# Performance work log

Measured on AMD Instinct MI355X. Metric: run time of the kernel, lower is better.

The kernel has to match this reference:

```python
import jax, jax.numpy as jnp
import numpy as np

E1 = 150000   # number of 1-hop edges
E2 = 150000   # number of 2-hop edges
T = 400000    # triangles per triangle class
C = 64        # in_channels
H = 64        # mlp_hidden_channels
L = 2         # num DR2FWL2Conv layers
N_MLP = 8     # MLPs per conv layer


def setup_inputs() -> dict:
    key = jax.random.key(0)
    ks = jax.random.split(key, 20)
    edge_attr = jax.random.normal(ks[0], (E1, C), jnp.float32)
    edge_attr2 = jax.random.normal(ks[1], (E2, C), jnp.float32)
    # triangle index tensors: rows (ij, ik, kj); hop type of each row decides the range
    triangle_1_1_1 = jax.random.randint(ks[2], (3, T), 0, E1)
    triangle_1_1_2 = jnp.stack([jax.random.randint(jax.random.fold_in(ks[3], r), (T,), 0, m)
                                for r, m in enumerate([E1, E1, E2])])
    triangle_1_2_2 = jnp.stack([jax.random.randint(jax.random.fold_in(ks[4], r), (T,), 0, m)
                                for r, m in enumerate([E1, E2, E2])])
    triangle_2_2_2 = jax.random.randint(ks[5], (3, T), 0, E2)
    inverse_edge_1 = jax.random.permutation(ks[6], E1)
    inverse_edge_2 = jax.random.permutation(ks[7], E2)
    s = 0.05
    mlp_w1 = jax.random.normal(ks[8], (L, N_MLP, C, H), jnp.float32) * s
    mlp_b1 = jnp.zeros((L, N_MLP, H), jnp.float32)
    mlp_w2 = jax.random.normal(ks[9], (L, N_MLP, H, C), jnp.float32) * s
    mlp_b2 = jnp.zeros((L, N_MLP, C), jnp.float32)
    lin_w1 = jax.random.normal(ks[10], (C, C), jnp.float32) * s
    lin_b1 = jnp.zeros((C,), jnp.float32)
    lin_w2 = jax.random.normal(ks[11], (C, C), jnp.float32) * s
    lin_b2 = jnp.zeros((C,), jnp.float32)
    return dict(edge_attr=edge_attr, edge_attr2=edge_attr2,
                triangle_1_1_1=triangle_1_1_1, triangle_1_1_2=triangle_1_1_2,
                triangle_1_2_2=triangle_1_2_2, triangle_2_2_2=triangle_2_2_2,
                inverse_edge_1=inverse_edge_1, inverse_edge_2=inverse_edge_2,
                mlp_w1=mlp_w1, mlp_b1=mlp_b1, mlp_w2=mlp_w2, mlp_b2=mlp_b2,
                lin_w1=lin_w1, lin_b1=lin_b1, lin_w2=lin_w2, lin_b2=lin_b2)


def reference(edge_attr, edge_attr2, triangle_1_1_1, triangle_1_1_2,
              triangle_1_2_2, triangle_2_2_2, inverse_edge_1, inverse_edge_2,
              mlp_w1, mlp_b1, mlp_w2, mlp_b2, lin_w1, lin_b1, lin_w2, lin_b2):
    eps = 0.0
    eps2 = 0.0
    ij111, ik111, kj111 = triangle_1_1_1
    ij112, ik112, kj112 = triangle_1_1_2
    ij122, ik122, kj122 = triangle_1_2_2
    ij222, ik222, kj222 = triangle_2_2_2
    seg = jax.ops.segment_sum

    e1, e2 = edge_attr, edge_attr2
    n1, n2 = e1.shape[0], e2.shape[0]
    for li in range(mlp_w1.shape[0]):
        def mlp(x, mi, li=li):
            h = jax.nn.relu(x @ mlp_w1[li, mi] + mlp_b1[li, mi])
            return h @ mlp_w2[li, mi] + mlp_b2[li, mi]
        m111 = seg(mlp(e1[ik111], 0) * mlp(e1[kj111], 0), ij111, num_segments=n1)
        m112 = seg(mlp(e1[ik112], 1) * mlp(e2[kj112], 2), ij112, num_segments=n1)
        m122 = seg(mlp(e2[ik122], 3) * mlp(e2[kj122], 3), ij122, num_segments=n1)
        e1 = e1 * (1.0 + eps) + m111 + m112 + m112[inverse_edge_1] + m122
        m211 = seg(mlp(e1[ij112], 4) * mlp(e1[ik112], 4), kj112, num_segments=n2)
        m212 = seg(mlp(e1[ij122], 5) * mlp(e2[kj122], 6), ik122, num_segments=n2)
        m222 = seg(mlp(e2[ik222], 7) * mlp(e2[kj222], 7), ij222, num_segments=n2)
        e2 = e2 * (1.0 + eps2) + m211 + m212 + m212[inverse_edge_2] + m222
        # norm=None (Identity), relu after, dropout=0 in eval
        e1, e2 = jax.nn.relu(e1), jax.nn.relu(e2)
    return (e1 @ lin_w1 + lin_b1, e2 @ lin_w2 + lin_b2)
```

## Files before the change

kernel.cpp:

```cpp
#include <hip/hip_runtime.h>
#include <hip/hip_fp16.h>


typedef unsigned short u16;
typedef unsigned int u32;
typedef _Float16 f16;
typedef __attribute__((ext_vector_type(8))) short s16x8;
typedef __attribute__((ext_vector_type(4))) float f32x4;
typedef __attribute__((ext_vector_type(8))) _Float16 f16x8;

#define MFMA16(a, b, c) __builtin_amdgcn_mfma_f32_16x16x32_bf16((a), (b), (c), 0, 0, 0)

static __device__ __forceinline__ u16 bf16_rne(float x) {
  u32 u = __float_as_uint(x);
  return (u16)((u + 0x7fffu + ((u >> 16) & 1u)) >> 16);
}
static __device__ __forceinline__ float bf16_f32(u16 h) {
  return __uint_as_float(((u32)h) << 16);
}
static __device__ __forceinline__ void cvt_hilo8_f16(const f16x8 v, s16x8& hi, s16x8& lo) {
#pragma unroll
  for (int j = 0; j < 8; j++) {
    float x = (float)v[j];
    u16 h = bf16_rne(x);
    hi[j] = (short)h;
    lo[j] = (short)bf16_rne(x - bf16_f32(h));
  }
}

__global__ __launch_bounds__(256) void repack_split_kernel(const float* __restrict__ src,
                                                           u16* __restrict__ hi, u16* __restrict__ lo, int nmat) {
  int o = blockIdx.x * 256 + threadIdx.x;
  int stride = gridDim.x * 256;
  int total = nmat * 4096;
  for (; o < total; o += stride) {
    int m = o >> 12, r = o & 4095;
    int j = r & 7, lane = (r >> 3) & 63, nt = (r >> 9) & 3, kt = (r >> 11) & 1;
    int k = kt * 32 + ((lane >> 4) << 3) + j;
    int n = nt * 16 + (lane & 15);
    float x = src[(size_t)m * 4096 + k * 64 + n];
    u16 h = bf16_rne(x);
    hi[o] = h;
    lo[o] = bf16_rne(x - bf16_f32(h));
  }
}

__global__ __launch_bounds__(256) void cvtcopy_kernel(const float* __restrict__ src, f16* __restrict__ dst, int n8) {
  int i = blockIdx.x * 256 + threadIdx.x;
  int stride = gridDim.x * 256;
  const f32x4* s4 = (const f32x4*)src;
  f16x8* d8 = (f16x8*)dst;
  for (; i < n8; i += stride) {
    f32x4 a = s4[2 * i], b = s4[2 * i + 1];
    f16x8 o;
#pragma unroll
    for (int j = 0; j < 4; j++) { o[j] = (f16)a[j]; o[4 + j] = (f16)b[j]; }
    d8[i] = o;
  }
}

__global__ __launch_bounds__(256) void relu16_kernel(f16* __restrict__ e, int n8) {
  int i = blockIdx.x * 256 + threadIdx.x;
  int stride = gridDim.x * 256;
  f16x8* e8 = (f16x8*)e;
  for (; i < n8; i += stride) {
    f16x8 v = e8[i];
#pragma unroll
    for (int j = 0; j < 8; j++) v[j] = v[j] > (f16)0 ? v[j] : (f16)0;
    e8[i] = v;
  }
}

template <bool DO_RELU>
__global__ __launch_bounds__(256) void addinvB_kernel(f16* __restrict__ e, const f16* __restrict__ B,
                                                      const int* __restrict__ inv, int E) {
  int i = blockIdx.x * 256 + threadIdx.x;
  int stride = gridDim.x * 256;
  int total = E * 8;
  f16x8* e8 = (f16x8*)e;
  const f16x8* B8 = (const f16x8*)B;
  for (; i < total; i += stride) {
    int r = i >> 3, q = i & 7;
    int ir = inv[r];
    f16x8 ev = e8[i];
    f16x8 bv = B8[i];
    f16x8 biv = B8[(size_t)ir * 8 + q];
#pragma unroll
    for (int j = 0; j < 8; j++) {
      float x = (float)ev[j] + (float)bv[j] + (float)biv[j];
      ev[j] = (f16)(DO_RELU ? fmaxf(x, 0.0f) : x);
    }
    e8[i] = ev;
  }
}

__global__ __launch_bounds__(256) void seg3_kernel(
    __half2* __restrict__ dstA, __half2* __restrict__ dstB,
    const __half2* __restrict__ paA, const __half2* __restrict__ pbA,
    const int* __restrict__ iA0, const int* __restrict__ iA1, const int* __restrict__ iA2,
    const __half2* __restrict__ paB, const __half2* __restrict__ pbB,
    const int* __restrict__ iB0, const int* __restrict__ iB1, const int* __restrict__ iB2,
    const __half2* __restrict__ paC, const __half2* __restrict__ pbC,
    const int* __restrict__ iC0, const int* __restrict__ iC1, const int* __restrict__ iC2,
    int T) {
  int i = blockIdx.x * 256 + threadIdx.x;
  int stride = gridDim.x * 256;
  int total = 3 * T * 32;
  for (; i < total; i += stride) {
    int u = i >> 5, cp = i & 31;
    __half2* dst;
    const __half2 *pa, *pb;
    const int *i0, *i1, *i2;
    int t;
    if (u < T) { t = u; dst = dstA; pa = paA; pb = pbA; i0 = iA0; i1 = iA1; i2 = iA2; }
    else if (u < 2 * T) { t = u - T; dst = dstB; pa = paB; pb = pbB; i0 = iB0; i1 = iB1; i2 = iB2; }
    else { t = u - 2 * T; dst = dstA; pa = paC; pb = pbC; i0 = iC0; i1 = iC1; i2 = iC2; }
    __half2 va = pa[(size_t)i1[t] * 32 + cp];
    __half2 vb = pb[(size_t)i2[t] * 32 + cp];
    float2 fa = __half22float2(va), fb = __half22float2(vb);
    __half2 prod = __floats2half2_rn(fa.x * fb.x, fa.y * fb.y);
    unsafeAtomicAdd(&dst[(size_t)i0[t] * 32 + cp], prod);
  }
}

__global__ __launch_bounds__(256) void mlpN_kernel(
    const f16* __restrict__ e1s, const f16* __restrict__ e2s,
    f16* __restrict__ d0, f16* __restrict__ d1, f16* __restrict__ d2,
    f16* __restrict__ d3, f16* __restrict__ d4, f16* __restrict__ d5,
    const u16* __restrict__ w1h_, const u16* __restrict__ w1l_,
    const u16* __restrict__ w2h_, const u16* __restrict__ w2l_,
    const float* __restrict__ b1_, const float* __restrict__ b2_,
    int miPacked, int selMask, int nUnits, int s1, int s2, int BPU) {
  __shared__ float hshm[4][1024];
  const int u = blockIdx.x / BPU;
  if (u >= nUnits) return;
  const int tid = threadIdx.x;
  const int wave = tid >> 6, lane = tid & 63;
  const int lrow = lane & 15, lk = lane >> 4;

  const int mi = (miPacked >> (4 * u)) & 15;
  const int sel = (selMask >> u) & 1;
  const f16* src = sel ? e2s : e1s;
  const int strips = sel ? s2 : s1;
  f16* dst = (u == 0) ? d0 : (u == 1) ? d1 : (u == 2) ? d2 : (u == 3) ? d3 : (u == 4) ? d4 : d5;

  const s16x8* W1H = (const s16x8*)(w1h_ + (size_t)mi * 4096);
  const s16x8* W1L = (const s16x8*)(w1l_ + (size_t)mi * 4096);
  const s16x8* W2H = (const s16x8*)(w2h_ + (size_t)mi * 4096);
  const s16x8* W2L = (const s16x8*)(w2l_ + (size_t)mi * 4096);
  s16x8 w1h[2][4], w1l[2][4], w2h[2][4], w2l[2][4];
#pragma unroll
  for (int kt = 0; kt < 2; kt++)
#pragma unroll
    for (int nt = 0; nt < 4; nt++) {
      const int f = (kt * 4 + nt) * 64 + lane;
      w1h[kt][nt] = W1H[f];
      w1l[kt][nt] = W1L[f];
      w2h[kt][nt] = W2H[f];
      w2l[kt][nt] = W2L[f];
    }
  float bias1[4], bias2[4];
#pragma unroll
  for (int nt = 0; nt < 4; nt++) {
    bias1[nt] = b1_[mi * 64 + nt * 16 + lrow];
    bias2[nt] = b2_[mi * 64 + nt * 16 + lrow];
  }

  float* hl = hshm[wave];
  const int lb = blockIdx.x % BPU;
  for (int strip = lb * 4 + wave; strip < strips; strip += BPU * 4) {
    const f16* xp = src + (size_t)(strip * 16 + lrow) * 64 + lk * 8;
    f16x8 xa = *(const f16x8*)(xp);
    f16x8 xb = *(const f16x8*)(xp + 32);
    s16x8 ah[2], al[2];
    cvt_hilo8_f16(xa, ah[0], al[0]);
    cvt_hilo8_f16(xb, ah[1], al[1]);

    f32x4 acc[4];
#pragma unroll
    for (int nt = 0; nt < 4; nt++) { acc[nt][0] = bias1[nt]; acc[nt][1] = bias1[nt]; acc[nt][2] = bias1[nt]; acc[nt][3] = bias1[nt]; }
#pragma unroll
    for (int kt = 0; kt < 2; kt++)
#pragma unroll
      for (int nt = 0; nt < 4; nt++) {
        acc[nt] = MFMA16(ah[kt], w1h[kt][nt], acc[nt]);
        acc[nt] = MFMA16(ah[kt], w1l[kt][nt], acc[nt]);
        acc[nt] = MFMA16(al[kt], w1h[kt][nt], acc[nt]);
      }

#pragma unroll
    for (int nt = 0; nt < 4; nt++)
#pragma unroll
      for (int r = 0; r < 4; r++) {
        const int row = lk * 4 + r;
        const int col = nt * 16 + lrow;
        hl[row * 64 + (col ^ ((row & 7) << 2))] = fmaxf(acc[nt][r], 0.0f);
      }
    s16x8 bh[2], bl[2];
#pragma unroll
    for (int kt = 0; kt < 2; kt++) {
      const int colb = kt * 32 + lk * 8;
      const int xr = (lrow & 7) << 2;
      f32x4 h0 = *(const f32x4*)&hl[lrow * 64 + ((colb + 0) ^ xr)];
      f32x4 h1 = *(const f32x4*)&hl[lrow * 64 + ((colb + 4) ^ xr)];
      s16x8 hi, lo;
#pragma unroll
      for (int j = 0; j < 4; j++) {
        float x = h0[j];
        u16 h = bf16_rne(x);
        hi[j] = (short)h; lo[j] = (short)bf16_rne(x - bf16_f32(h));
      }
#pragma unroll
      for (int j = 0; j < 4; j++) {
        float x = h1[j];
        u16 h = bf16_rne(x);
        hi[4 + j] = (short)h; lo[4 + j] = (short)bf16_rne(x - bf16_f32(h));
      }
      bh[kt] = hi; bl[kt] = lo;
    }

    f32x4 out[4];
#pragma unroll
    for (int nt = 0; nt < 4; nt++) { out[nt][0] = bias2[nt]; out[nt][1] = bias2[nt]; out[nt][2] = bias2[nt]; out[nt][3] = bias2[nt]; }
#pragma unroll
    for (int kt = 0; kt < 2; kt++)
#pragma unroll
      for (int nt = 0; nt < 4; nt++) {
        out[nt] = MFMA16(bh[kt], w2h[kt][nt], out[nt]);
        out[nt] = MFMA16(bh[kt], w2l[kt][nt], out[nt]);
        out[nt] = MFMA16(bl[kt], w2h[kt][nt], out[nt]);
      }

    f16* dp = dst + (size_t)strip * 1024;
#pragma unroll
    for (int nt = 0; nt < 4; nt++)
#pragma unroll
      for (int r = 0; r < 4; r++)
        dp[(lk * 4 + r) * 64 + nt * 16 + lrow] = (f16)out[nt][r];
  }
}

template <bool RELU>
__global__ __launch_bounds__(256) void lin_kernel(const f16* __restrict__ src, float* __restrict__ dst,
                                                  const u16* __restrict__ wh_, const u16* __restrict__ wl_,
                                                  const float* __restrict__ b_, int nstrips) {
  const int tid = threadIdx.x;
  const int wave = tid >> 6, lane = tid & 63;
  const int lrow = lane & 15, lk = lane >> 4;

  const s16x8* WH = (const s16x8*)wh_;
  const s16x8* WL = (const s16x8*)wl_;
  s16x8 wh[2][4], wl[2][4];
#pragma unroll
  for (int kt = 0; kt < 2; kt++)
#pragma unroll
    for (int nt = 0; nt < 4; nt++) {
      const int f = (kt * 4 + nt) * 64 + lane;
      wh[kt][nt] = WH[f];
      wl[kt][nt] = WL[f];
    }
  float bias[4];
#pragma unroll
  for (int nt = 0; nt < 4; nt++) bias[nt] = b_[nt * 16 + lrow];

  for (int s = blockIdx.x * 4 + wave; s < nstrips; s += gridDim.x * 4) {
    const f16* xp = src + (size_t)(s * 16 + lrow) * 64 + lk * 8;
    f16x8 xa = *(const f16x8*)(xp);
    f16x8 xb = *(const f16x8*)(xp + 32);
    if (RELU) {
#pragma unroll
      for (int j = 0; j < 8; j++) {
        xa[j] = xa[j] > (f16)0 ? xa[j] : (f16)0;
        xb[j] = xb[j] > (f16)0 ? xb[j] : (f16)0;
      }
    }
    s16x8 ah[2], al[2];
    cvt_hilo8_f16(xa, ah[0], al[0]);
    cvt_hilo8_f16(xb, ah[1], al[1]);

    f32x4 acc[4];
#pragma unroll
    for (int nt = 0; nt < 4; nt++) { acc[nt][0] = bias[nt]; acc[nt][1] = bias[nt]; acc[nt][2] = bias[nt]; acc[nt][3] = bias[nt]; }
#pragma unroll
    for (int kt = 0; kt < 2; kt++)
#pragma unroll
      for (int nt = 0; nt < 4; nt++) {
        acc[nt] = MFMA16(ah[kt], wh[kt][nt], acc[nt]);
        acc[nt] = MFMA16(ah[kt], wl[kt][nt], acc[nt]);
        acc[nt] = MFMA16(al[kt], wh[kt][nt], acc[nt]);
      }
    float* dp = dst + (size_t)s * 1024;
#pragma unroll
    for (int nt = 0; nt < 4; nt++)
#pragma unroll
      for (int r = 0; r < 4; r++)
        dp[(lk * 4 + r) * 64 + nt * 16 + lrow] = acc[nt][r];
  }
}

extern "C" void kernel_launch(void* const* d_in, const int* in_sizes, int n_in,
                              void* d_out, int out_size, void* d_ws, size_t ws_size,
                              hipStream_t stream) {
  const float* in_e1 = (const float*)d_in[0];
  const float* in_e2 = (const float*)d_in[1];
  const int* t111 = (const int*)d_in[2];
  const int* t112 = (const int*)d_in[3];
  const int* t122 = (const int*)d_in[4];
  const int* t222 = (const int*)d_in[5];
  const int* inv1 = (const int*)d_in[6];
  const int* inv2 = (const int*)d_in[7];
  const float* mw1 = (const float*)d_in[8];
  const float* mb1 = (const float*)d_in[9];
  const float* mw2 = (const float*)d_in[10];
  const float* mb2 = (const float*)d_in[11];
  const float* lw1 = (const float*)d_in[12];
  const float* lb1 = (const float*)d_in[13];
  const float* lw2 = (const float*)d_in[14];
  const float* lb2 = (const float*)d_in[15];

  const int E1 = in_sizes[0] / 64, E2 = in_sizes[1] / 64;
  const int T = in_sizes[2] / 3;
  const int L = in_sizes[8] / (8 * 64 * 64);
  const size_t nE1 = (size_t)E1 * 64, nE2 = (size_t)E2 * 64;
  const size_t nMax = nE1 > nE2 ? nE1 : nE2;

  f16* e1b = (f16*)d_ws;
  f16* e2b = e1b + nE1;
  f16* mB = e2b + nE2;
  f16* q0 = mB + nMax;
  f16* q1 = q0 + nE1;
  const size_t wmat = (size_t)L * 8 * 4096;
  u16* w1h = (u16*)(q1 + nE1);
  u16* w1l = w1h + wmat;
  u16* w2h = w1l + wmat;
  u16* w2l = w2h + wmat;
  u16* lwh = w2l + wmat;
  u16* lwl = lwh + 8192;
  const size_t needB = (nE1 + nE2 + nMax + 2 * nE1) * 2 + (4 * wmat + 4 * 4096) * 2 + 64;
  if (ws_size < needB) return;

  f16* q2 = (f16*)d_out;
  f16* q3 = q2 + nE2;
  f16* q6 = q3 + nE2;
  f16* q7 = q6 + nE2;
  f16* q4 = q0;
  f16* q5 = q1;

  const int s1 = E1 / 16, s2 = E2 / 16;
  const int SEGB = 2048, ELTB = 2048, BPU = 256, LINB = 256;

  repack_split_kernel<<<256, 256, 0, stream>>>(mw1, w1h, w1l, L * 8);
  repack_split_kernel<<<256, 256, 0, stream>>>(mw2, w2h, w2l, L * 8);
  repack_split_kernel<<<32, 256, 0, stream>>>(lw1, lwh, lwl, 1);
  repack_split_kernel<<<32, 256, 0, stream>>>(lw2, lwh + 4096, lwl + 4096, 1);
  cvtcopy_kernel<<<ELTB, 256, 0, stream>>>(in_e1, e1b, (int)(nE1 / 8));
  cvtcopy_kernel<<<ELTB, 256, 0, stream>>>(in_e2, e2b, (int)(nE2 / 8));

  for (int li = 0; li < L; li++) {
    const u16* W1H = w1h + (size_t)li * 8 * 4096;
    const u16* W1L = w1l + (size_t)li * 8 * 4096;
    const u16* W2H = w2h + (size_t)li * 8 * 4096;
    const u16* W2L = w2l + (size_t)li * 8 * 4096;
    const float* B1 = mb1 + (size_t)li * 8 * 64;
    const float* B2 = mb2 + (size_t)li * 8 * 64;

    mlpN_kernel<<<6 * BPU, 256, 0, stream>>>(e1b, e2b, q0, q1, q2, q3, q6, q7,
                                             W1H, W1L, W2H, W2L, B1, B2,
                                             0x763210, 0x3C, 6, s1, s2, BPU);
    hipMemsetAsync(mB, 0, nE1 * 2, stream);
    seg3_kernel<<<SEGB, 256, 0, stream>>>(
        (__half2*)e1b, (__half2*)mB,
        (const __half2*)q0, (const __half2*)q0, t111, t111 + T, t111 + 2 * T,
        (const __half2*)q1, (const __half2*)q2, t112, t112 + T, t112 + 2 * T,
        (const __half2*)q3, (const __half2*)q3, t122, t122 + T, t122 + 2 * T, T);
    addinvB_kernel<false><<<ELTB, 256, 0, stream>>>(e1b, mB, inv1, E1);

    mlpN_kernel<<<2 * BPU, 256, 0, stream>>>(e1b, e2b, q4, q5, q2, q3, q6, q7,
                                             W1H, W1L, W2H, W2L, B1, B2,
                                             0x54, 0x0, 2, s1, s2, BPU);
    if (li < L - 1) relu16_kernel<<<ELTB, 256, 0, stream>>>(e1b, (int)(nE1 / 8));

    hipMemsetAsync(mB, 0, nE2 * 2, stream);
    seg3_kernel<<<SEGB, 256, 0, stream>>>(
        (__half2*)e2b, (__half2*)mB,
        (const __half2*)q4, (const __half2*)q4, t112 + 2 * T, t112, t112 + T,
        (const __half2*)q5, (const __half2*)q6, t122 + T, t122, t122 + 2 * T,
        (const __half2*)q7, (const __half2*)q7, t222, t222 + T, t222 + 2 * T, T);
    addinvB_kernel<true><<<ELTB, 256, 0, stream>>>(e2b, mB, inv2, E2);
  }

  lin_kernel<true><<<LINB, 256, 0, stream>>>(e1b, (float*)d_out, lwh, lwl, lb1, s1);
  lin_kernel<false><<<LINB, 256, 0, stream>>>(e2b, (float*)d_out + nE1, lwh + 4096, lwl + 4096, lb2, s2);
}
```

Measured before the change: 818.6 us.

## Bucket triangles by destination and accumulate segment sums in shared memory

Replaces the global fp16 atomic scatter-add segment kernel with a counting-sort preprocessing step (histogram, single-block scan, scatter) that groups triangles by 32-row destination buckets into packed 64-bit payloads. A new per-bucket kernel accumulates products in fp32 shared-memory atomics and writes results once, removing the memset and global atomic contention. It adds preprocessing kernels each call, a serial single-block scan, and small 64-thread blocks with possible load imbalance across buckets.

```diff
diff --git a/kernel.cpp b/kernel.cpp
--- a/kernel.cpp
+++ b/kernel.cpp
@@ -4,6 +4,7 @@
 
 typedef unsigned short u16;
 typedef unsigned int u32;
+typedef unsigned long long u64;
 typedef _Float16 f16;
 typedef __attribute__((ext_vector_type(8))) short s16x8;
 typedef __attribute__((ext_vector_type(4))) float f32x4;
@@ -25,6 +26,134 @@
     u16 h = bf16_rne(x);
     hi[j] = (short)h;
     lo[j] = (short)bf16_rne(x - bf16_f32(h));
+  }
+}
+
+static __device__ __forceinline__ void class_ptrs(int c, const int* t111, const int* t112,
+                                                  const int* t122, const int* t222, int T,
+                                                  const int*& D, const int*& A, const int*& B) {
+  switch (c) {
+    case 0: D = t111;          A = t111 + T; B = t111 + 2 * T; break;
+    case 1: D = t112;          A = t112 + T; B = t112 + 2 * T; break;
+    case 2: D = t122;          A = t122 + T; B = t122 + 2 * T; break;
+    case 3: D = t112 + 2 * T;  A = t112;     B = t112 + T;     break;
+    case 4: D = t122 + T;      A = t122;     B = t122 + 2 * T; break;
+    default: D = t222;         A = t222 + T; B = t222 + 2 * T; break;
+  }
+}
+static __device__ __forceinline__ int cls_ofs(int c, int NB1, int NB2) {
+  return (c < 3) ? c * NB1 : 3 * NB1 + (c - 3) * NB2;
+}
+
+__global__ __launch_bounds__(256) void hist_kernel(int* __restrict__ cnt,
+                                                   const int* t111, const int* t112,
+                                                   const int* t122, const int* t222,
+                                                   int T, int NB1, int NB2) {
+  int i = blockIdx.x * 256 + threadIdx.x;
+  if (i >= 6 * T) return;
+  int c = i / T, t = i - c * T;
+  const int *D, *A, *B;
+  class_ptrs(c, t111, t112, t122, t222, T, D, A, B);
+  atomicAdd(&cnt[cls_ofs(c, NB1, NB2) + (D[t] >> 5)], 1);
+}
+
+__global__ __launch_bounds__(1024) void scan_kernel(const int* __restrict__ cnt, int* __restrict__ boff,
+                                                    int* __restrict__ pos, int CNT) {
+  __shared__ int sh[1024];
+  __shared__ int carry;
+  int tid = threadIdx.x;
+  if (tid == 0) carry = 0;
+  __syncthreads();
+  for (int base0 = 0; base0 < CNT; base0 += 1024) {
+    int i = base0 + tid;
+    int v = (i < CNT) ? cnt[i] : 0;
+    sh[tid] = v;
+    __syncthreads();
+    for (int off = 1; off < 1024; off <<= 1) {
+      int x = (tid >= off) ? sh[tid - off] : 0;
+      __syncthreads();
+      sh[tid] += x;
+      __syncthreads();
+    }
+    int incl = sh[tid];
+    int cbase = carry;
+    if (i < CNT) { boff[i] = cbase + incl - v; pos[i] = cbase + incl - v; }
+    __syncthreads();
+    if (tid == 1023) carry = cbase + incl;
+    __syncthreads();
+  }
+  if (tid == 0) boff[CNT] = carry;
+}
+
+__global__ __launch_bounds__(256) void scatter_kernel(int* __restrict__ pos, u64* __restrict__ payload,
+                                                      const int* t111, const int* t112,
+                                                      const int* t122, const int* t222,
+                                                      int T, int NB1, int NB2) {
+  int i = blockIdx.x * 256 + threadIdx.x;
+  if (i >= 6 * T) return;
+  int c = i / T, t = i - c * T;
+  const int *D, *A, *B;
+  class_ptrs(c, t111, t112, t122, t222, T, D, A, B);
+  int d = D[t];
+  int slot = atomicAdd(&pos[cls_ofs(c, NB1, NB2) + (d >> 5)], 1);
+  payload[slot] = (u64)(u32)A[t] | ((u64)(u32)B[t] << 20) | ((u64)(d & 31) << 40);
+}
+
+__global__ __launch_bounds__(64) void segbkt_kernel(
+    __half2* __restrict__ e, __half2* __restrict__ mB,
+    const u64* __restrict__ payload, const int* __restrict__ boff,
+    int ofsA, int ofsB, int ofsC,
+    const __half2* __restrict__ paA, const __half2* __restrict__ pbA,
+    const __half2* __restrict__ paB, const __half2* __restrict__ pbB,
+    const __half2* __restrict__ paC, const __half2* __restrict__ pbC,
+    int E) {
+  __shared__ float accE[32 * 64];
+  __shared__ float accM[32 * 64];
+  const int b = blockIdx.x;
+  const int tid = threadIdx.x;
+  const int h = tid >> 5;
+  const int cl = tid & 31;
+#pragma unroll
+  for (int i = 0; i < 32; i++) {
+    accE[i * 64 + tid] = 0.0f;
+    accM[i * 64 + tid] = 0.0f;
+  }
+  __syncthreads();
+
+#pragma unroll
+  for (int k = 0; k < 3; k++) {
+    const int ofs = (k == 0) ? ofsA : (k == 1) ? ofsB : ofsC;
+    const __half2* pa = (k == 0) ? paA : (k == 1) ? paB : paC;
+    const __half2* pb = (k == 0) ? pbA : (k == 1) ? pbB : pbC;
+    float* acc = (k == 1) ? accM : accE;
+    const int t0 = boff[ofs + b], t1 = boff[ofs + b + 1];
+    for (int t = t0 + h; t < t1; t += 2) {
+      u64 p = payload[t];
+      int ia = (int)(p & 0xFFFFF);
+      int ib = (int)((p >> 20) & 0xFFFFF);
+      int dlo = (int)(p >> 40);
+      float2 a = __half22float2(pa[(size_t)ia * 32 + cl]);
+      float2 v = __half22float2(pb[(size_t)ib * 32 + cl]);
+      atomicAdd(&acc[dlo * 64 + 2 * cl], a.x * v.x);
+      atomicAdd(&acc[dlo * 64 + 2 * cl + 1], a.y * v.y);
+    }
+  }
+  __syncthreads();
+
+  const int rbase = b * 32;
+#pragma unroll
+  for (int it = 0; it < 16; it++) {
+    int idx = it * 64 + tid;
+    int row = idx >> 5, cp = idx & 31;
+    int grow = rbase + row;
+    if (grow < E) {
+      size_t g = (size_t)grow * 32 + cp;
+      float2 ae = make_float2(accE[row * 64 + 2 * cp], accE[row * 64 + 2 * cp + 1]);
+      float2 am = make_float2(accM[row * 64 + 2 * cp], accM[row * 64 + 2 * cp + 1]);
+      float2 ev = __half22float2(e[g]);
+      e[g] = __floats2half2_rn(ev.x + ae.x, ev.y + ae.y);
+      mB[g] = __floats2half2_rn(am.x, am.y);
+    }
   }
 }
 
@@ -94,35 +223,6 @@
   }
 }
 
-__global__ __launch_bounds__(256) void seg3_kernel(
-    __half2* __restrict__ dstA, __half2* __restrict__ dstB,
-    const __half2* __restrict__ paA, const __half2* __restrict__ pbA,
-    const int* __restrict__ iA0, const int* __restrict__ iA1, const int* __restrict__ iA2,
-    const __half2* __restrict__ paB, const __half2* __restrict__ pbB,
-    const int* __restrict__ iB0, const int* __restrict__ iB1, const int* __restrict__ iB2,
-    const __half2* __restrict__ paC, const __half2* __restrict__ pbC,
-    const int* __restrict__ iC0, const int* __restrict__ iC1, const int* __restrict__ iC2,
-    int T) {
-  int i = blockIdx.x * 256 + threadIdx.x;
-  int stride = gridDim.x * 256;
-  int total = 3 * T * 32;
-  for (; i < total; i += stride) {
-    int u = i >> 5, cp = i & 31;
-    __half2* dst;
-    const __half2 *pa, *pb;
-    const int *i0, *i1, *i2;
-    int t;
-    if (u < T) { t = u; dst = dstA; pa = paA; pb = pbA; i0 = iA0; i1 = iA1; i2 = iA2; }
-    else if (u < 2 * T) { t = u - T; dst = dstB; pa = paB; pb = pbB; i0 = iB0; i1 = iB1; i2 = iB2; }
-    else { t = u - 2 * T; dst = dstA; pa = paC; pb = pbC; i0 = iC0; i1 = iC1; i2 = iC2; }
-    __half2 va = pa[(size_t)i1[t] * 32 + cp];
-    __half2 vb = pb[(size_t)i2[t] * 32 + cp];
-    float2 fa = __half22float2(va), fb = __half22float2(vb);
-    __half2 prod = __floats2half2_rn(fa.x * fb.x, fa.y * fb.y);
-    unsafeAtomicAdd(&dst[(size_t)i0[t] * 32 + cp], prod);
-  }
-}
-
 __global__ __launch_bounds__(256) void mlpN_kernel(
     const f16* __restrict__ e1s, const f16* __restrict__ e2s,
     f16* __restrict__ d0, f16* __restrict__ d1, f16* __restrict__ d2,
@@ -207,14 +307,14 @@
 #pragma unroll
       for (int j = 0; j < 4; j++) {
         float x = h0[j];
-        u16 h = bf16_rne(x);
-        hi[j] = (short)h; lo[j] = (short)bf16_rne(x - bf16_f32(h));
+        u16 hh = bf16_rne(x);
+        hi[j] = (short)hh; lo[j] = (short)bf16_rne(x - bf16_f32(hh));
       }
 #pragma unroll
       for (int j = 0; j < 4; j++) {
         float x = h1[j];
-        u16 h = bf16_rne(x);
-        hi[4 + j] = (short)h; lo[4 + j] = (short)bf16_rne(x - bf16_f32(h));
+        u16 hh = bf16_rne(x);
+        hi[4 + j] = (short)hh; lo[4 + j] = (short)bf16_rne(x - bf16_f32(hh));
       }
       bh[kt] = hi; bl[kt] = lo;
     }
@@ -323,20 +423,26 @@
   const int L = in_sizes[8] / (8 * 64 * 64);
   const size_t nE1 = (size_t)E1 * 64, nE2 = (size_t)E2 * 64;
   const size_t nMax = nE1 > nE2 ? nE1 : nE2;
+  const int NB1 = (E1 + 31) / 32, NB2 = (E2 + 31) / 32;
+  const int CNT = 3 * NB1 + 3 * NB2;
 
   f16* e1b = (f16*)d_ws;
   f16* e2b = e1b + nE1;
   f16* mB = e2b + nE2;
   f16* q0 = mB + nMax;
   f16* q1 = q0 + nE1;
+  u64* payload = (u64*)(q1 + nE1);
   const size_t wmat = (size_t)L * 8 * 4096;
-  u16* w1h = (u16*)(q1 + nE1);
+  u16* w1h = (u16*)(payload + (size_t)6 * T);
   u16* w1l = w1h + wmat;
   u16* w2h = w1l + wmat;
   u16* w2l = w2h + wmat;
   u16* lwh = w2l + wmat;
   u16* lwl = lwh + 8192;
-  const size_t needB = (nE1 + nE2 + nMax + 2 * nE1) * 2 + (4 * wmat + 4 * 4096) * 2 + 64;
+  int* cnt = (int*)(lwl + 8192);
+  int* boff = cnt + CNT;
+  int* pos = boff + CNT + 1;
+  const size_t needB = (char*)(pos + CNT) - (char*)d_ws + 64;
   if (ws_size < needB) return;
 
   f16* q2 = (f16*)d_out;
@@ -347,7 +453,13 @@
   f16* q5 = q1;
 
   const int s1 = E1 / 16, s2 = E2 / 16;
-  const int SEGB = 2048, ELTB = 2048, BPU = 256, LINB = 256;
+  const int ELTB = 2048, BPU = 256, LINB = 256;
+  const int triB = (6 * T + 255) / 256;
+
+  hipMemsetAsync(cnt, 0, (size_t)CNT * 4, stream);
+  hist_kernel<<<triB, 256, 0, stream>>>(cnt, t111, t112, t122, t222, T, NB1, NB2);
+  scan_kernel<<<1, 1024, 0, stream>>>(cnt, boff, pos, CNT);
+  scatter_kernel<<<triB, 256, 0, stream>>>(pos, payload, t111, t112, t122, t222, T, NB1, NB2);
 
   repack_split_kernel<<<256, 256, 0, stream>>>(mw1, w1h, w1l, L * 8);
   repack_split_kernel<<<256, 256, 0, stream>>>(mw2, w2h, w2l, L * 8);
@@ -367,12 +479,12 @@
     mlpN_kernel<<<6 * BPU, 256, 0, stream>>>(e1b, e2b, q0, q1, q2, q3, q6, q7,
                                              W1H, W1L, W2H, W2L, B1, B2,
                                              0x763210, 0x3C, 6, s1, s2, BPU);
-    hipMemsetAsync(mB, 0, nE1 * 2, stream);
-    seg3_kernel<<<SEGB, 256, 0, stream>>>(
-        (__half2*)e1b, (__half2*)mB,
-        (const __half2*)q0, (const __half2*)q0, t111, t111 + T, t111 + 2 * T,
-        (const __half2*)q1, (const __half2*)q2, t112, t112 + T, t112 + 2 * T,
-        (const __half2*)q3, (const __half2*)q3, t122, t122 + T, t122 + 2 * T, T);
+    segbkt_kernel<<<NB1, 64, 0, stream>>>(
+        (__half2*)e1b, (__half2*)mB, payload, boff,
+        0 * NB1, 1 * NB1, 2 * NB1,
+        (const __half2*)q0, (const __half2*)q0,
+        (const __half2*)q1, (const __half2*)q2,
+        (const __half2*)q3, (const __half2*)q3, E1);
     addinvB_kernel<false><<<ELTB, 256, 0, stream>>>(e1b, mB, inv1, E1);
 
     mlpN_kernel<<<2 * BPU, 256, 0, stream>>>(e1b, e2b, q4, q5, q2, q3, q6, q7,
@@ -380,12 +492,12 @@
                                              0x54, 0x0, 2, s1, s2, BPU);
     if (li < L - 1) relu16_kernel<<<ELTB, 256, 0, stream>>>(e1b, (int)(nE1 / 8));
 
-    hipMemsetAsync(mB, 0, nE2 * 2, stream);
-    seg3_kernel<<<SEGB, 256, 0, stream>>>(
-        (__half2*)e2b, (__half2*)mB,
-        (const __half2*)q4, (const __half2*)q4, t112 + 2 * T, t112, t112 + T,
-        (const __half2*)q5, (const __half2*)q6, t122 + T, t122, t122 + 2 * T,
-        (const __half2*)q7, (const __half2*)q7, t222, t222 + T, t222 + 2 * T, T);
+    segbkt_kernel<<<NB2, 64, 0, stream>>>(
+        (__half2*)e2b, (__half2*)mB, payload, boff,
+        3 * NB1, 3 * NB1 + NB2, 3 * NB1 + 2 * NB2,
+        (const __half2*)q4, (const __half2*)q4,
+        (const __half2*)q5, (const __half2*)q6,
+        (const __half2*)q7, (const __half2*)q7, E2);
     addinvB_kernel<true><<<ELTB, 256, 0, stream>>>(e2b, mB, inv2, E2);
   }
 
```

Result: slower. 2.380 ms (+190.7%).
